# Kernel optimization log

Measured on AMD Instinct MI355X. Metric: run time of the kernel, lower is better.

The kernel has to match this reference:

```python
import jax, jax.numpy as jnp
import numpy as np

B, L, H, HEADS, BLOCKS = 4, 256, 256, 4, 2
D = H // HEADS
EPS = 1e-8
NEG = -4294967295.0  # -2**32 + 1


def rmsnorm(x, w):
    return x * jax.lax.rsqrt(jnp.mean(x * x, axis=-1, keepdims=True) + EPS) * w


def split_heads(x):  # [B,L,H] -> [h,B,L,d]
    return x.reshape(B, L, HEADS, D).transpose(2, 0, 1, 3)


def split_heads_tm(x):  # [B,L,L,H] -> [h,B,L,L,d]
    return x.reshape(B, L, L, HEADS, D).transpose(3, 0, 1, 2, 4)


def setup_inputs() -> dict:
    key = jax.random.key(0)
    ks = jax.random.split(key, 24)
    s = 0.02
    inp = {
        "seqs": jax.random.normal(ks[0], (B, L, H), jnp.float32),
        "attention_mask": jnp.triu(jnp.ones((L, L), jnp.bool_), k=1),  # causal: True = masked
        "timeline_mask": jnp.zeros((B, L), jnp.bool_),
        "time_matrix_K": jax.random.normal(ks[1], (B, L, L, H), jnp.float32),
        "time_matrix_V": jax.random.normal(ks[2], (B, L, L, H), jnp.float32),
        "abs_pos_K": jax.random.normal(ks[3], (B, L, H), jnp.float32),
        "abs_pos_V": jax.random.normal(ks[4], (B, L, H), jnp.float32),
        # parameters, stacked over blocks
        "ln_attn": jnp.ones((BLOCKS, H), jnp.float32),
        "Qw": jax.random.normal(ks[5], (BLOCKS, H, H), jnp.float32) * s,
        "Qb": jnp.zeros((BLOCKS, H), jnp.float32),
        "Kw": jax.random.normal(ks[6], (BLOCKS, H, H), jnp.float32) * s,
        "Kb": jnp.zeros((BLOCKS, H), jnp.float32),
        "Vw": jax.random.normal(ks[7], (BLOCKS, H, H), jnp.float32) * s,
        "Vb": jnp.zeros((BLOCKS, H), jnp.float32),
        "ln_ffn": jnp.ones((BLOCKS, H), jnp.float32),
        "W1": jax.random.normal(ks[8], (BLOCKS, H, H), jnp.float32) * s,
        "b1": jnp.zeros((BLOCKS, H), jnp.float32),
        "W2": jax.random.normal(ks[9], (BLOCKS, H, H), jnp.float32) * s,
        "b2": jnp.zeros((BLOCKS, H), jnp.float32),
        "ln_last": jnp.ones((H,), jnp.float32),
    }
    return inp


def reference(seqs, attention_mask, timeline_mask, time_matrix_K, time_matrix_V,
              abs_pos_K, abs_pos_V, ln_attn, Qw, Qb, Kw, Kb, Vw, Vb,
              ln_ffn, W1, b1, W2, b2, ln_last):
    tmK = split_heads_tm(time_matrix_K)           # [h,B,L,L,d]
    tmV = split_heads_tm(time_matrix_V)
    apK = split_heads(abs_pos_K)                  # [h,B,L,d]
    apV = split_heads(abs_pos_V)
    # True = masked; time_mask masks padded query rows, attn_mask is causal
    mask = timeline_mask[None, :, :, None] | attention_mask[None, None, :, :]  # [1,B,L,L]
    scale = 1.0 / jnp.sqrt(jnp.float32(D))
    not_pad = 1.0 - timeline_mask.astype(seqs.dtype)[:, :, None]  # [B,L,1]

    for i in range(BLOCKS):
        x = rmsnorm(seqs, ln_attn[i])
        Q = split_heads(x @ Qw[i].T + Qb[i])      # queries from normed x
        K = split_heads(seqs @ Kw[i].T + Kb[i])   # keys/values from raw seqs
        V = split_heads(seqs @ Vw[i].T + Vb[i])
        w = jnp.einsum('hbqd,hbkd->hbqk', Q, K)
        w += jnp.einsum('hbqd,hbkd->hbqk', Q, apK)
        w += jnp.einsum('hbqkd,hbqd->hbqk', tmK, Q)
        w = jnp.where(mask, NEG, w * scale)
        A = jax.nn.softmax(w, axis=-1)            # [h,B,L,L]
        out = jnp.einsum('hbqk,hbkd->hbqd', A, V)
        out += jnp.einsum('hbqk,hbkd->hbqd', A, apV)
        out += jnp.einsum('hbqk,hbqkd->hbqd', A, tmV)
        out = out.transpose(1, 2, 0, 3).reshape(B, L, H)  # merge heads
        seqs = seqs + out
        h2 = rmsnorm(seqs, ln_ffn[i])
        ffn = jax.nn.relu(h2 @ W1[i].T + b1[i]) @ W2[i].T + b2[i]
        seqs = (seqs + ffn) * not_pad
    return rmsnorm(seqs, ln_last)
```

## Files before the change

### kernel.cpp

```cpp
#include <hip/hip_runtime.h>
#include <math.h>

#define LLEN 256
#define HDIM 256
#define MM 1024
#define NEGV -4294967295.0f

__device__ __forceinline__ void gemm_core(
    float* A_s, float* W_s, float* r_s,
    const float* __restrict__ A, const float* __restrict__ ln,
    const float* __restrict__ W, const float* __restrict__ bias,
    const float* __restrict__ addv, const float* __restrict__ resid,
    const unsigned char* __restrict__ tl, float* __restrict__ C,
    int relu, int m0, int n0)
{
    int t = threadIdx.x;
    int srow = t >> 4, sc4 = t & 15;
    int tm = t >> 4, tn = t & 15;
    float acc[2][4];
    #pragma unroll
    for (int i = 0; i < 2; ++i)
        #pragma unroll
        for (int j = 0; j < 4; ++j) acc[i][j] = 0.f;
    float ssq[2] = {0.f, 0.f};

    for (int kc = 0; kc < HDIM; kc += 64) {
        #pragma unroll
        for (int i = 0; i < 2; ++i) {
            int row = srow + 16 * i;
            float4 va = *(const float4*)&A[(size_t)(m0 + row) * HDIM + kc + sc4 * 4];
            ssq[i] += va.x*va.x + va.y*va.y + va.z*va.z + va.w*va.w;
            if (ln) {
                va.x *= ln[kc + sc4*4 + 0]; va.y *= ln[kc + sc4*4 + 1];
                va.z *= ln[kc + sc4*4 + 2]; va.w *= ln[kc + sc4*4 + 3];
            }
            *(float4*)&A_s[row * 68 + sc4 * 4] = va;
        }
        #pragma unroll
        for (int i = 0; i < 4; ++i) {
            int row = srow + 16 * i;
            *(float4*)&W_s[row * 68 + sc4 * 4] =
                *(const float4*)&W[(size_t)(n0 + row) * HDIM + kc + sc4 * 4];
        }
        __syncthreads();
        #pragma unroll 4
        for (int k4 = 0; k4 < 16; ++k4) {
            float4 a0 = *(const float4*)&A_s[(2*tm + 0) * 68 + k4 * 4];
            float4 a1 = *(const float4*)&A_s[(2*tm + 1) * 68 + k4 * 4];
            #pragma unroll
            for (int j = 0; j < 4; ++j) {
                float4 wv = *(const float4*)&W_s[(tn + 16*j) * 68 + k4 * 4];
                acc[0][j] = fmaf(a0.x, wv.x, fmaf(a0.y, wv.y,
                            fmaf(a0.z, wv.z, fmaf(a0.w, wv.w, acc[0][j]))));
                acc[1][j] = fmaf(a1.x, wv.x, fmaf(a1.y, wv.y,
                            fmaf(a1.z, wv.z, fmaf(a1.w, wv.w, acc[1][j]))));
            }
        }
        __syncthreads();
    }

    if (ln) {
        #pragma unroll
        for (int i = 0; i < 2; ++i) {
            float v = ssq[i];
            v += __shfl_xor(v, 1); v += __shfl_xor(v, 2);
            v += __shfl_xor(v, 4); v += __shfl_xor(v, 8);
            if (sc4 == 0) r_s[srow + 16 * i] = rsqrtf(v * (1.0f / HDIM) + 1e-8f);
        }
        __syncthreads();
    }

    #pragma unroll
    for (int i = 0; i < 2; ++i) {
        int row = m0 + 2*tm + i;
        float rr = ln ? r_s[2*tm + i] : 1.0f;
        float tlf = tl ? (tl[row] ? 0.f : 1.f) : 1.f;
        #pragma unroll
        for (int j = 0; j < 4; ++j) {
            int col = n0 + tn + 16*j;
            float v = acc[i][j] * rr + bias[col];
            if (relu) v = fmaxf(v, 0.f);
            size_t idx = (size_t)row * HDIM + col;
            if (addv)  v += addv[idx];
            if (resid) v += resid[idx];
            v *= tlf;
            C[idx] = v;
        }
    }
}

__global__ __launch_bounds__(256) void qkv_kernel(
    const float* __restrict__ s, const float* __restrict__ ln_attn,
    const float* __restrict__ Qw, const float* __restrict__ Qb,
    const float* __restrict__ Kw, const float* __restrict__ Kb,
    const float* __restrict__ Vw, const float* __restrict__ Vb,
    const float* __restrict__ apK, const float* __restrict__ apV,
    float* __restrict__ qb, float* __restrict__ kb, float* __restrict__ vb)
{
    __shared__ __align__(16) float A_s[32 * 68];
    __shared__ __align__(16) float W_s[64 * 68];
    __shared__ float r_s[32];
    int m0 = blockIdx.x * 32;
    int sel = blockIdx.y >> 2;
    int n0 = (blockIdx.y & 3) * 64;
    if (sel == 0)
        gemm_core(A_s, W_s, r_s, s, ln_attn, Qw, Qb, nullptr, nullptr, nullptr, qb, 0, m0, n0);
    else if (sel == 1)
        gemm_core(A_s, W_s, r_s, s, nullptr, Kw, Kb, apK, nullptr, nullptr, kb, 0, m0, n0);
    else
        gemm_core(A_s, W_s, r_s, s, nullptr, Vw, Vb, apV, nullptr, nullptr, vb, 0, m0, n0);
}

__global__ __launch_bounds__(256) void gemm_kernel(
    const float* __restrict__ A, const float* __restrict__ ln,
    const float* __restrict__ W, const float* __restrict__ bias,
    const float* __restrict__ resid, const unsigned char* __restrict__ tl,
    float* __restrict__ C, int relu)
{
    __shared__ __align__(16) float A_s[32 * 68];
    __shared__ __align__(16) float W_s[64 * 68];
    __shared__ float r_s[32];
    gemm_core(A_s, W_s, r_s, A, ln, W, bias, nullptr, resid, tl, C, relu,
              blockIdx.x * 32, blockIdx.y * 64);
}

__global__ __launch_bounds__(1024, 8) void attn_kernel(
    const float* __restrict__ Q, const float* __restrict__ Kp,
    const float* __restrict__ Vp, const float* __restrict__ tmK,
    const float* __restrict__ tmV, const unsigned char* __restrict__ tl,
    float* __restrict__ s)
{
    int g = blockIdx.x;
    int b = g >> 7, p = g & 127;
    int tid = threadIdx.x;
    int w = tid >> 6, lane = tid & 63;
    int hh = lane >> 4;

    __shared__ float w_s[4][257];
    __shared__ __align__(16) float out_s[16][256];

    const float4* Kp4 = (const float4*)(Kp + (size_t)b * LLEN * HDIM);
    const float4* Vp4 = (const float4*)(Vp + (size_t)b * LLEN * HDIM);

    for (int rr = 0; rr < 2; ++rr) {
        int q = rr ? (255 - p) : p;
        int bq = b * 256 + q;
        float4 qf = ((const float4*)(Q + (size_t)bq * HDIM))[lane];
        bool tlq = tl[bq] != 0;
        int kmax = tlq ? (LLEN - 1) : q;

        const float4* tmK4 = (const float4*)(tmK + (size_t)bq * LLEN * HDIM);
        const float4* tmV4 = (const float4*)(tmV + (size_t)bq * LLEN * HDIM);

        for (int k = w; k <= kmax; k += 16) {
            float4 kv = Kp4[k * 64 + lane];
            float4 tv = tmK4[k * 64 + lane];
            float sc = qf.x * (kv.x + tv.x) + qf.y * (kv.y + tv.y)
                     + qf.z * (kv.z + tv.z) + qf.w * (kv.w + tv.w);
            sc += __shfl_xor(sc, 1);
            sc += __shfl_xor(sc, 2);
            sc += __shfl_xor(sc, 4);
            sc += __shfl_xor(sc, 8);
            if ((lane & 15) == 0) w_s[lane >> 4][k] = sc;
        }
        __syncthreads();

        if (w < 4) {
            float v0 = w_s[w][lane],       v1 = w_s[w][lane + 64];
            float v2 = w_s[w][lane + 128], v3 = w_s[w][lane + 192];
            v0 = (tlq || (lane       > q)) ? NEGV : v0 * 0.125f;
            v1 = (tlq || (lane + 64  > q)) ? NEGV : v1 * 0.125f;
            v2 = (tlq || (lane + 128 > q)) ? NEGV : v2 * 0.125f;
            v3 = (tlq || (lane + 192 > q)) ? NEGV : v3 * 0.125f;
            float mx = fmaxf(fmaxf(v0, v1), fmaxf(v2, v3));
            #pragma unroll
            for (int m2 = 1; m2 < 64; m2 <<= 1) mx = fmaxf(mx, __shfl_xor(mx, m2));
            float e0 = __expf(v0 - mx), e1 = __expf(v1 - mx);
            float e2 = __expf(v2 - mx), e3 = __expf(v3 - mx);
            float sm = e0 + e1 + e2 + e3;
            #pragma unroll
            for (int m2 = 1; m2 < 64; m2 <<= 1) sm += __shfl_xor(sm, m2);
            float inv = 1.0f / sm;
            w_s[w][lane] = e0 * inv;       w_s[w][lane + 64] = e1 * inv;
            w_s[w][lane + 128] = e2 * inv; w_s[w][lane + 192] = e3 * inv;
        }
        __syncthreads();

        float4 acc = {0.f, 0.f, 0.f, 0.f};
        for (int k = w; k <= kmax; k += 16) {
            float a = w_s[hh][k];
            float4 vv = Vp4[k * 64 + lane];
            float4 tv = tmV4[k * 64 + lane];
            acc.x = fmaf(a, vv.x + tv.x, acc.x);
            acc.y = fmaf(a, vv.y + tv.y, acc.y);
            acc.z = fmaf(a, vv.z + tv.z, acc.z);
            acc.w = fmaf(a, vv.w + tv.w, acc.w);
        }
        *(float4*)&out_s[w][lane * 4] = acc;
        __syncthreads();

        if (tid < 256) {
            float pp = 0.f;
            #pragma unroll
            for (int j = 0; j < 16; ++j) pp += out_s[j][tid];
            s[(size_t)bq * HDIM + tid] += pp;
        }
        __syncthreads();
    }
}

__global__ __launch_bounds__(256) void rmsnorm_kernel(
    const float* __restrict__ x, const float* __restrict__ w, float* __restrict__ y)
{
    int row = blockIdx.x;
    int tid = threadIdx.x;
    float v = x[(size_t)row * HDIM + tid];
    float ss = v * v;
    #pragma unroll
    for (int m = 1; m < 64; m <<= 1) ss += __shfl_xor(ss, m);
    __shared__ float red[4];
    if ((tid & 63) == 0) red[tid >> 6] = ss;
    __syncthreads();
    float tot = red[0] + red[1] + red[2] + red[3];
    float r = rsqrtf(tot * (1.0f / HDIM) + 1e-8f);
    y[(size_t)row * HDIM + tid] = v * r * w[tid];
}

extern "C" void kernel_launch(void* const* d_in, const int* in_sizes, int n_in,
                              void* d_out, int out_size, void* d_ws, size_t ws_size,
                              hipStream_t stream)
{
    const float* seqs = (const float*)d_in[0];
    const unsigned char* tl = (const unsigned char*)d_in[2];
    const float* tmK = (const float*)d_in[3];
    const float* tmV = (const float*)d_in[4];
    const float* apK = (const float*)d_in[5];
    const float* apV = (const float*)d_in[6];
    const float* ln_attn = (const float*)d_in[7];
    const float* Qw = (const float*)d_in[8];
    const float* Qb = (const float*)d_in[9];
    const float* Kw = (const float*)d_in[10];
    const float* Kb = (const float*)d_in[11];
    const float* Vw = (const float*)d_in[12];
    const float* Vb = (const float*)d_in[13];
    const float* ln_ffn = (const float*)d_in[14];
    const float* W1 = (const float*)d_in[15];
    const float* b1 = (const float*)d_in[16];
    const float* W2 = (const float*)d_in[17];
    const float* b2 = (const float*)d_in[18];
    const float* ln_last = (const float*)d_in[19];
    float* out = (float*)d_out;

    const size_t NROW = (size_t)MM * HDIM;
    float* s  = (float*)d_ws;
    float* qb = s  + NROW;
    float* kb = qb + NROW;
    float* vb = kb + NROW;
    float* tb = vb + NROW;

    hipMemcpyAsync(s, seqs, NROW * sizeof(float), hipMemcpyDeviceToDevice, stream);

    for (int i = 0; i < 2; ++i) {
        const float* Qwi = Qw + (size_t)i * HDIM * HDIM;
        const float* Kwi = Kw + (size_t)i * HDIM * HDIM;
        const float* Vwi = Vw + (size_t)i * HDIM * HDIM;
        const float* W1i = W1 + (size_t)i * HDIM * HDIM;
        const float* W2i = W2 + (size_t)i * HDIM * HDIM;

        qkv_kernel<<<dim3(32, 12), 256, 0, stream>>>(
            s, ln_attn + i * HDIM, Qwi, Qb + i * HDIM, Kwi, Kb + i * HDIM,
            Vwi, Vb + i * HDIM, apK, apV, qb, kb, vb);
        attn_kernel<<<512, 1024, 0, stream>>>(qb, kb, vb, tmK, tmV, tl, s);
        gemm_kernel<<<dim3(32, 4), 256, 0, stream>>>(
            s, ln_ffn + i * HDIM, W1i, b1 + i * HDIM, nullptr, nullptr, tb, 1);
        gemm_kernel<<<dim3(32, 4), 256, 0, stream>>>(
            tb, nullptr, W2i, b2 + i * HDIM, s, tl, s, 0);
    }
    rmsnorm_kernel<<<MM, 256, 0, stream>>>(s, ln_last, out);
}
```

Before: 210.8 us.

## Merge attention query pair phases, prefetch K/V loads, enlarge GEMM tiles, drop seqs copy

The attention kernel now processes both paired queries' score passes together with a single softmax phase and fewer barriers. Its K/tmK and V/tmV loops software-prefetch the next row so loads overlap compute. The GEMM tile grows from 32x64 to 64x64 with a 4x4 per-thread micro-tile, raising register reuse but halving block count. The initial device-to-device copy of seqs is removed by reading the input directly on the first block and writing attention output to a separate destination.

```diff
diff --git a/kernel.cpp b/kernel.cpp
--- a/kernel.cpp
+++ b/kernel.cpp
@@ -17,16 +17,16 @@
     int t = threadIdx.x;
     int srow = t >> 4, sc4 = t & 15;
     int tm = t >> 4, tn = t & 15;
-    float acc[2][4];
-    #pragma unroll
-    for (int i = 0; i < 2; ++i)
+    float acc[4][4];
+    #pragma unroll
+    for (int i = 0; i < 4; ++i)
         #pragma unroll
         for (int j = 0; j < 4; ++j) acc[i][j] = 0.f;
-    float ssq[2] = {0.f, 0.f};
+    float ssq[4] = {0.f, 0.f, 0.f, 0.f};
 
     for (int kc = 0; kc < HDIM; kc += 64) {
         #pragma unroll
-        for (int i = 0; i < 2; ++i) {
+        for (int i = 0; i < 4; ++i) {
             int row = srow + 16 * i;
             float4 va = *(const float4*)&A[(size_t)(m0 + row) * HDIM + kc + sc4 * 4];
             ssq[i] += va.x*va.x + va.y*va.y + va.z*va.z + va.w*va.w;
@@ -35,33 +35,32 @@
                 va.z *= ln[kc + sc4*4 + 2]; va.w *= ln[kc + sc4*4 + 3];
             }
             *(float4*)&A_s[row * 68 + sc4 * 4] = va;
-        }
-        #pragma unroll
-        for (int i = 0; i < 4; ++i) {
-            int row = srow + 16 * i;
             *(float4*)&W_s[row * 68 + sc4 * 4] =
                 *(const float4*)&W[(size_t)(n0 + row) * HDIM + kc + sc4 * 4];
         }
         __syncthreads();
         #pragma unroll 4
         for (int k4 = 0; k4 < 16; ++k4) {
-            float4 a0 = *(const float4*)&A_s[(2*tm + 0) * 68 + k4 * 4];
-            float4 a1 = *(const float4*)&A_s[(2*tm + 1) * 68 + k4 * 4];
+            float4 a[4], wv[4];
             #pragma unroll
-            for (int j = 0; j < 4; ++j) {
-                float4 wv = *(const float4*)&W_s[(tn + 16*j) * 68 + k4 * 4];
-                acc[0][j] = fmaf(a0.x, wv.x, fmaf(a0.y, wv.y,
-                            fmaf(a0.z, wv.z, fmaf(a0.w, wv.w, acc[0][j]))));
-                acc[1][j] = fmaf(a1.x, wv.x, fmaf(a1.y, wv.y,
-                            fmaf(a1.z, wv.z, fmaf(a1.w, wv.w, acc[1][j]))));
-            }
+            for (int i = 0; i < 4; ++i)
+                a[i] = *(const float4*)&A_s[(4*tm + i) * 68 + k4 * 4];
+            #pragma unroll
+            for (int j = 0; j < 4; ++j)
+                wv[j] = *(const float4*)&W_s[(tn + 16*j) * 68 + k4 * 4];
+            #pragma unroll
+            for (int i = 0; i < 4; ++i)
+                #pragma unroll
+                for (int j = 0; j < 4; ++j)
+                    acc[i][j] = fmaf(a[i].x, wv[j].x, fmaf(a[i].y, wv[j].y,
+                                fmaf(a[i].z, wv[j].z, fmaf(a[i].w, wv[j].w, acc[i][j]))));
         }
         __syncthreads();
     }
 
     if (ln) {
         #pragma unroll
-        for (int i = 0; i < 2; ++i) {
+        for (int i = 0; i < 4; ++i) {
             float v = ssq[i];
             v += __shfl_xor(v, 1); v += __shfl_xor(v, 2);
             v += __shfl_xor(v, 4); v += __shfl_xor(v, 8);
@@ -71,9 +70,9 @@
     }
 
     #pragma unroll
-    for (int i = 0; i < 2; ++i) {
-        int row = m0 + 2*tm + i;
-        float rr = ln ? r_s[2*tm + i] : 1.0f;
+    for (int i = 0; i < 4; ++i) {
+        int row = m0 + 4*tm + i;
+        float rr = ln ? r_s[4*tm + i] : 1.0f;
         float tlf = tl ? (tl[row] ? 0.f : 1.f) : 1.f;
         #pragma unroll
         for (int j = 0; j < 4; ++j) {
@@ -97,10 +96,10 @@
     const float* __restrict__ apK, const float* __restrict__ apV,
     float* __restrict__ qb, float* __restrict__ kb, float* __restrict__ vb)
 {
-    __shared__ __align__(16) float A_s[32 * 68];
+    __shared__ __align__(16) float A_s[64 * 68];
     __shared__ __align__(16) float W_s[64 * 68];
-    __shared__ float r_s[32];
-    int m0 = blockIdx.x * 32;
+    __shared__ float r_s[64];
+    int m0 = blockIdx.x * 64;
     int sel = blockIdx.y >> 2;
     int n0 = (blockIdx.y & 3) * 64;
     if (sel == 0)
@@ -117,18 +116,18 @@
     const float* __restrict__ resid, const unsigned char* __restrict__ tl,
     float* __restrict__ C, int relu)
 {
-    __shared__ __align__(16) float A_s[32 * 68];
+    __shared__ __align__(16) float A_s[64 * 68];
     __shared__ __align__(16) float W_s[64 * 68];
-    __shared__ float r_s[32];
+    __shared__ float r_s[64];
     gemm_core(A_s, W_s, r_s, A, ln, W, bias, nullptr, resid, tl, C, relu,
-              blockIdx.x * 32, blockIdx.y * 64);
+              blockIdx.x * 64, blockIdx.y * 64);
 }
 
 __global__ __launch_bounds__(1024, 8) void attn_kernel(
     const float* __restrict__ Q, const float* __restrict__ Kp,
     const float* __restrict__ Vp, const float* __restrict__ tmK,
     const float* __restrict__ tmV, const unsigned char* __restrict__ tl,
-    float* __restrict__ s)
+    const float* __restrict__ src, float* __restrict__ dst)
 {
     int g = blockIdx.x;
     int b = g >> 7, p = g & 127;
@@ -136,76 +135,121 @@
     int w = tid >> 6, lane = tid & 63;
     int hh = lane >> 4;
 
-    __shared__ float w_s[4][257];
+    __shared__ float w_s[2][4][257];
     __shared__ __align__(16) float out_s[16][256];
+
+    int q0 = p, q1 = 255 - p;
+    int bq0 = b * 256 + q0, bq1 = b * 256 + q1;
+    float4 qf0 = ((const float4*)(Q + (size_t)bq0 * HDIM))[lane];
+    float4 qf1 = ((const float4*)(Q + (size_t)bq1 * HDIM))[lane];
+    bool tl0 = tl[bq0] != 0, tl1 = tl[bq1] != 0;
+    int kmax0 = tl0 ? (LLEN - 1) : q0;
+    int kmax1 = tl1 ? (LLEN - 1) : q1;
 
     const float4* Kp4 = (const float4*)(Kp + (size_t)b * LLEN * HDIM);
     const float4* Vp4 = (const float4*)(Vp + (size_t)b * LLEN * HDIM);
-
+    const float4* tmK0 = (const float4*)(tmK + (size_t)bq0 * LLEN * HDIM);
+    const float4* tmK1 = (const float4*)(tmK + (size_t)bq1 * LLEN * HDIM);
+    const float4* tmV0 = (const float4*)(tmV + (size_t)bq0 * LLEN * HDIM);
+    const float4* tmV1 = (const float4*)(tmV + (size_t)bq1 * LLEN * HDIM);
+
+    #pragma unroll
     for (int rr = 0; rr < 2; ++rr) {
-        int q = rr ? (255 - p) : p;
-        int bq = b * 256 + q;
-        float4 qf = ((const float4*)(Q + (size_t)bq * HDIM))[lane];
-        bool tlq = tl[bq] != 0;
-        int kmax = tlq ? (LLEN - 1) : q;
-
-        const float4* tmK4 = (const float4*)(tmK + (size_t)bq * LLEN * HDIM);
-        const float4* tmV4 = (const float4*)(tmV + (size_t)bq * LLEN * HDIM);
-
-        for (int k = w; k <= kmax; k += 16) {
+        int kmax = rr ? kmax1 : kmax0;
+        const float4* tmK4 = rr ? tmK1 : tmK0;
+        float4 qf = rr ? qf1 : qf0;
+        int k = w;
+        if (k <= kmax) {
             float4 kv = Kp4[k * 64 + lane];
             float4 tv = tmK4[k * 64 + lane];
-            float sc = qf.x * (kv.x + tv.x) + qf.y * (kv.y + tv.y)
-                     + qf.z * (kv.z + tv.z) + qf.w * (kv.w + tv.w);
-            sc += __shfl_xor(sc, 1);
-            sc += __shfl_xor(sc, 2);
-            sc += __shfl_xor(sc, 4);
-            sc += __shfl_xor(sc, 8);
-            if ((lane & 15) == 0) w_s[lane >> 4][k] = sc;
-        }
-        __syncthreads();
-
-        if (w < 4) {
-            float v0 = w_s[w][lane],       v1 = w_s[w][lane + 64];
-            float v2 = w_s[w][lane + 128], v3 = w_s[w][lane + 192];
-            v0 = (tlq || (lane       > q)) ? NEGV : v0 * 0.125f;
-            v1 = (tlq || (lane + 64  > q)) ? NEGV : v1 * 0.125f;
-            v2 = (tlq || (lane + 128 > q)) ? NEGV : v2 * 0.125f;
-            v3 = (tlq || (lane + 192 > q)) ? NEGV : v3 * 0.125f;
-            float mx = fmaxf(fmaxf(v0, v1), fmaxf(v2, v3));
-            #pragma unroll
-            for (int m2 = 1; m2 < 64; m2 <<= 1) mx = fmaxf(mx, __shfl_xor(mx, m2));
-            float e0 = __expf(v0 - mx), e1 = __expf(v1 - mx);
-            float e2 = __expf(v2 - mx), e3 = __expf(v3 - mx);
-            float sm = e0 + e1 + e2 + e3;
-            #pragma unroll
-            for (int m2 = 1; m2 < 64; m2 <<= 1) sm += __shfl_xor(sm, m2);
-            float inv = 1.0f / sm;
-            w_s[w][lane] = e0 * inv;       w_s[w][lane + 64] = e1 * inv;
-            w_s[w][lane + 128] = e2 * inv; w_s[w][lane + 192] = e3 * inv;
-        }
-        __syncthreads();
-
+            while (true) {
+                int kn = k + 16;
+                bool more = (kn <= kmax);
+                float4 kv2, tv2;
+                if (more) { kv2 = Kp4[kn * 64 + lane]; tv2 = tmK4[kn * 64 + lane]; }
+                float sc = qf.x * (kv.x + tv.x) + qf.y * (kv.y + tv.y)
+                         + qf.z * (kv.z + tv.z) + qf.w * (kv.w + tv.w);
+                sc += __shfl_xor(sc, 1);
+                sc += __shfl_xor(sc, 2);
+                sc += __shfl_xor(sc, 4);
+                sc += __shfl_xor(sc, 8);
+                if ((lane & 15) == 0) w_s[rr][lane >> 4][k] = sc;
+                if (!more) break;
+                kv = kv2; tv = tv2; k = kn;
+            }
+        }
+    }
+    __syncthreads();
+
+    if (w < 8) {
+        int r = w >> 2, h = w & 3;
+        int q = r ? q1 : q0;
+        bool tlq = r ? tl1 : tl0;
+        float v0 = w_s[r][h][lane],       v1 = w_s[r][h][lane + 64];
+        float v2 = w_s[r][h][lane + 128], v3 = w_s[r][h][lane + 192];
+        v0 = (tlq || (lane       > q)) ? NEGV : v0 * 0.125f;
+        v1 = (tlq || (lane + 64  > q)) ? NEGV : v1 * 0.125f;
+        v2 = (tlq || (lane + 128 > q)) ? NEGV : v2 * 0.125f;
+        v3 = (tlq || (lane + 192 > q)) ? NEGV : v3 * 0.125f;
+        float mx = fmaxf(fmaxf(v0, v1), fmaxf(v2, v3));
+        #pragma unroll
+        for (int m2 = 1; m2 < 64; m2 <<= 1) mx = fmaxf(mx, __shfl_xor(mx, m2));
+        float e0 = __expf(v0 - mx), e1 = __expf(v1 - mx);
+        float e2 = __expf(v2 - mx), e3 = __expf(v3 - mx);
+        float sm = e0 + e1 + e2 + e3;
+        #pragma unroll
+        for (int m2 = 1; m2 < 64; m2 <<= 1) sm += __shfl_xor(sm, m2);
+        float inv = 1.0f / sm;
+        w_s[r][h][lane] = e0 * inv;       w_s[r][h][lane + 64] = e1 * inv;
+        w_s[r][h][lane + 128] = e2 * inv; w_s[r][h][lane + 192] = e3 * inv;
+    }
+    __syncthreads();
+
+    float4 acc0 = {0.f, 0.f, 0.f, 0.f}, acc1 = {0.f, 0.f, 0.f, 0.f};
+    #pragma unroll
+    for (int rr = 0; rr < 2; ++rr) {
+        int kmax = rr ? kmax1 : kmax0;
+        const float4* tmV4 = rr ? tmV1 : tmV0;
         float4 acc = {0.f, 0.f, 0.f, 0.f};
-        for (int k = w; k <= kmax; k += 16) {
-            float a = w_s[hh][k];
+        int k = w;
+        if (k <= kmax) {
             float4 vv = Vp4[k * 64 + lane];
             float4 tv = tmV4[k * 64 + lane];
-            acc.x = fmaf(a, vv.x + tv.x, acc.x);
-            acc.y = fmaf(a, vv.y + tv.y, acc.y);
-            acc.z = fmaf(a, vv.z + tv.z, acc.z);
-            acc.w = fmaf(a, vv.w + tv.w, acc.w);
-        }
-        *(float4*)&out_s[w][lane * 4] = acc;
-        __syncthreads();
-
-        if (tid < 256) {
-            float pp = 0.f;
-            #pragma unroll
-            for (int j = 0; j < 16; ++j) pp += out_s[j][tid];
-            s[(size_t)bq * HDIM + tid] += pp;
-        }
-        __syncthreads();
+            while (true) {
+                int kn = k + 16;
+                bool more = (kn <= kmax);
+                float4 vv2, tv2;
+                if (more) { vv2 = Vp4[kn * 64 + lane]; tv2 = tmV4[kn * 64 + lane]; }
+                float a = w_s[rr][hh][k];
+                acc.x = fmaf(a, vv.x + tv.x, acc.x);
+                acc.y = fmaf(a, vv.y + tv.y, acc.y);
+                acc.z = fmaf(a, vv.z + tv.z, acc.z);
+                acc.w = fmaf(a, vv.w + tv.w, acc.w);
+                if (!more) break;
+                vv = vv2; tv = tv2; k = kn;
+            }
+        }
+        if (rr) acc1 = acc; else acc0 = acc;
+    }
+
+    *(float4*)&out_s[w][lane * 4] = acc0;
+    __syncthreads();
+    if (tid < 256) {
+        float pp = 0.f;
+        #pragma unroll
+        for (int j = 0; j < 16; ++j) pp += out_s[j][tid];
+        size_t idx = (size_t)bq0 * HDIM + tid;
+        dst[idx] = src[idx] + pp;
+    }
+    __syncthreads();
+    *(float4*)&out_s[w][lane * 4] = acc1;
+    __syncthreads();
+    if (tid < 256) {
+        float pp = 0.f;
+        #pragma unroll
+        for (int j = 0; j < 16; ++j) pp += out_s[j][tid];
+        size_t idx = (size_t)bq1 * HDIM + tid;
+        dst[idx] = src[idx] + pp;
     }
 }
 
@@ -258,22 +302,21 @@
     float* vb = kb + NROW;
     float* tb = vb + NROW;
 
-    hipMemcpyAsync(s, seqs, NROW * sizeof(float), hipMemcpyDeviceToDevice, stream);
-
     for (int i = 0; i < 2; ++i) {
         const float* Qwi = Qw + (size_t)i * HDIM * HDIM;
         const float* Kwi = Kw + (size_t)i * HDIM * HDIM;
         const float* Vwi = Vw + (size_t)i * HDIM * HDIM;
         const float* W1i = W1 + (size_t)i * HDIM * HDIM;
         const float* W2i = W2 + (size_t)i * HDIM * HDIM;
-
-        qkv_kernel<<<dim3(32, 12), 256, 0, stream>>>(
-            s, ln_attn + i * HDIM, Qwi, Qb + i * HDIM, Kwi, Kb + i * HDIM,
+        const float* cur = (i == 0) ? seqs : s;
+
+        qkv_kernel<<<dim3(16, 12), 256, 0, stream>>>(
+            cur, ln_attn + i * HDIM, Qwi, Qb + i * HDIM, Kwi, Kb + i * HDIM,
             Vwi, Vb + i * HDIM, apK, apV, qb, kb, vb);
-        attn_kernel<<<512, 1024, 0, stream>>>(qb, kb, vb, tmK, tmV, tl, s);
-        gemm_kernel<<<dim3(32, 4), 256, 0, stream>>>(
+        attn_kernel<<<512, 1024, 0, stream>>>(qb, kb, vb, tmK, tmV, tl, cur, s);
+        gemm_kernel<<<dim3(16, 4), 256, 0, stream>>>(
             s, ln_ffn + i * HDIM, W1i, b1 + i * HDIM, nullptr, nullptr, tb, 1);
-        gemm_kernel<<<dim3(32, 4), 256, 0, stream>>>(
+        gemm_kernel<<<dim3(16, 4), 256, 0, stream>>>(
             tb, nullptr, W2i, b2 + i * HDIM, s, tl, s, 0);
     }
     rmsnorm_kernel<<<MM, 256, 0, stream>>>(s, ln_last, out);
```

New measurement: 238.3 us. 13.0% more time.

## Fuse attention score and value passes with online softmax per warp

Applied to the files above, without the earlier changes.

Replaces the two-pass attention (scores, then a block-wide softmax, then a separate V pass) with a single pass. Each warp keeps a running max and sum (online softmax) and accumulates V plus time-matrix V in the same loop, and per-warp partials are merged at the end with rescaling. This removes a block barrier and a second sweep over K/V indices, and lets the tmK and tmV loads be issued together. It also drops the initial device-to-device copy by reading the input sequence directly in block 0 and writing the residual into the workspace. The cost is extra exp calls per key.

```diff
diff --git a/kernel.cpp b/kernel.cpp
--- a/kernel.cpp
+++ b/kernel.cpp
@@ -128,7 +128,7 @@
     const float* __restrict__ Q, const float* __restrict__ Kp,
     const float* __restrict__ Vp, const float* __restrict__ tmK,
     const float* __restrict__ tmV, const unsigned char* __restrict__ tl,
-    float* __restrict__ s)
+    const float* __restrict__ src, float* __restrict__ dst)
 {
     int g = blockIdx.x;
     int b = g >> 7, p = g & 127;
@@ -136,12 +136,13 @@
     int w = tid >> 6, lane = tid & 63;
     int hh = lane >> 4;
 
-    __shared__ float w_s[4][257];
     __shared__ __align__(16) float out_s[16][256];
+    __shared__ float m_s[16][4], l_s[16][4];
 
     const float4* Kp4 = (const float4*)(Kp + (size_t)b * LLEN * HDIM);
     const float4* Vp4 = (const float4*)(Vp + (size_t)b * LLEN * HDIM);
 
+    #pragma unroll
     for (int rr = 0; rr < 2; ++rr) {
         int q = rr ? (255 - p) : p;
         int bq = b * 256 + q;
@@ -152,58 +153,51 @@
         const float4* tmK4 = (const float4*)(tmK + (size_t)bq * LLEN * HDIM);
         const float4* tmV4 = (const float4*)(tmV + (size_t)bq * LLEN * HDIM);
 
+        float4 acc = {0.f, 0.f, 0.f, 0.f};
+        float m = -INFINITY, l = 0.f;
+
         for (int k = w; k <= kmax; k += 16) {
-            float4 kv = Kp4[k * 64 + lane];
-            float4 tv = tmK4[k * 64 + lane];
-            float sc = qf.x * (kv.x + tv.x) + qf.y * (kv.y + tv.y)
-                     + qf.z * (kv.z + tv.z) + qf.w * (kv.w + tv.w);
-            sc += __shfl_xor(sc, 1);
-            sc += __shfl_xor(sc, 2);
-            sc += __shfl_xor(sc, 4);
-            sc += __shfl_xor(sc, 8);
-            if ((lane & 15) == 0) w_s[lane >> 4][k] = sc;
-        }
-        __syncthreads();
-
-        if (w < 4) {
-            float v0 = w_s[w][lane],       v1 = w_s[w][lane + 64];
-            float v2 = w_s[w][lane + 128], v3 = w_s[w][lane + 192];
-            v0 = (tlq || (lane       > q)) ? NEGV : v0 * 0.125f;
-            v1 = (tlq || (lane + 64  > q)) ? NEGV : v1 * 0.125f;
-            v2 = (tlq || (lane + 128 > q)) ? NEGV : v2 * 0.125f;
-            v3 = (tlq || (lane + 192 > q)) ? NEGV : v3 * 0.125f;
-            float mx = fmaxf(fmaxf(v0, v1), fmaxf(v2, v3));
+            int off = k * 64 + lane;
+            float4 kv = Kp4[off];
+            float4 tv = tmK4[off];
+            float4 vv = Vp4[off];
+            float4 tw = tmV4[off];
+            float s = qf.x * (kv.x + tv.x) + qf.y * (kv.y + tv.y)
+                    + qf.z * (kv.z + tv.z) + qf.w * (kv.w + tv.w);
+            s += __shfl_xor(s, 1);
+            s += __shfl_xor(s, 2);
+            s += __shfl_xor(s, 4);
+            s += __shfl_xor(s, 8);
+            s = tlq ? NEGV : s * 0.125f;
+            float mn = fmaxf(m, s);
+            float c = __expf(m - mn);
+            float e = __expf(s - mn);
+            l = l * c + e;
+            acc.x = fmaf(acc.x, c, e * (vv.x + tw.x));
+            acc.y = fmaf(acc.y, c, e * (vv.y + tw.y));
+            acc.z = fmaf(acc.z, c, e * (vv.z + tw.z));
+            acc.w = fmaf(acc.w, c, e * (vv.w + tw.w));
+            m = mn;
+        }
+
+        if ((lane & 15) == 0) { m_s[w][hh] = m; l_s[w][hh] = l; }
+        *(float4*)&out_s[w][lane * 4] = acc;
+        __syncthreads();
+
+        if (tid < 256) {
+            int h = tid >> 6;
+            float mt = -INFINITY;
             #pragma unroll
-            for (int m2 = 1; m2 < 64; m2 <<= 1) mx = fmaxf(mx, __shfl_xor(mx, m2));
-            float e0 = __expf(v0 - mx), e1 = __expf(v1 - mx);
-            float e2 = __expf(v2 - mx), e3 = __expf(v3 - mx);
-            float sm = e0 + e1 + e2 + e3;
+            for (int j = 0; j < 16; ++j) mt = fmaxf(mt, m_s[j][h]);
+            float lt = 0.f, o = 0.f;
             #pragma unroll
-            for (int m2 = 1; m2 < 64; m2 <<= 1) sm += __shfl_xor(sm, m2);
-            float inv = 1.0f / sm;
-            w_s[w][lane] = e0 * inv;       w_s[w][lane + 64] = e1 * inv;
-            w_s[w][lane + 128] = e2 * inv; w_s[w][lane + 192] = e3 * inv;
-        }
-        __syncthreads();
-
-        float4 acc = {0.f, 0.f, 0.f, 0.f};
-        for (int k = w; k <= kmax; k += 16) {
-            float a = w_s[hh][k];
-            float4 vv = Vp4[k * 64 + lane];
-            float4 tv = tmV4[k * 64 + lane];
-            acc.x = fmaf(a, vv.x + tv.x, acc.x);
-            acc.y = fmaf(a, vv.y + tv.y, acc.y);
-            acc.z = fmaf(a, vv.z + tv.z, acc.z);
-            acc.w = fmaf(a, vv.w + tv.w, acc.w);
-        }
-        *(float4*)&out_s[w][lane * 4] = acc;
-        __syncthreads();
-
-        if (tid < 256) {
-            float pp = 0.f;
-            #pragma unroll
-            for (int j = 0; j < 16; ++j) pp += out_s[j][tid];
-            s[(size_t)bq * HDIM + tid] += pp;
+            for (int j = 0; j < 16; ++j) {
+                float f = __expf(m_s[j][h] - mt);
+                lt = fmaf(l_s[j][h], f, lt);
+                o  = fmaf(out_s[j][tid], f, o);
+            }
+            size_t idx = (size_t)bq * HDIM + tid;
+            dst[idx] = src[idx] + o / lt;
         }
         __syncthreads();
     }
@@ -258,19 +252,18 @@
     float* vb = kb + NROW;
     float* tb = vb + NROW;
 
-    hipMemcpyAsync(s, seqs, NROW * sizeof(float), hipMemcpyDeviceToDevice, stream);
-
     for (int i = 0; i < 2; ++i) {
         const float* Qwi = Qw + (size_t)i * HDIM * HDIM;
         const float* Kwi = Kw + (size_t)i * HDIM * HDIM;
         const float* Vwi = Vw + (size_t)i * HDIM * HDIM;
         const float* W1i = W1 + (size_t)i * HDIM * HDIM;
         const float* W2i = W2 + (size_t)i * HDIM * HDIM;
+        const float* cur = (i == 0) ? seqs : s;
 
         qkv_kernel<<<dim3(32, 12), 256, 0, stream>>>(
-            s, ln_attn + i * HDIM, Qwi, Qb + i * HDIM, Kwi, Kb + i * HDIM,
+            cur, ln_attn + i * HDIM, Qwi, Qb + i * HDIM, Kwi, Kb + i * HDIM,
             Vwi, Vb + i * HDIM, apK, apV, qb, kb, vb);
-        attn_kernel<<<512, 1024, 0, stream>>>(qb, kb, vb, tmK, tmV, tl, s);
+        attn_kernel<<<512, 1024, 0, stream>>>(qb, kb, vb, tmK, tmV, tl, cur, s);
         gemm_kernel<<<dim3(32, 4), 256, 0, stream>>>(
             s, ln_ffn + i * HDIM, W1i, b1 + i * HDIM, nullptr, nullptr, tb, 1);
         gemm_kernel<<<dim3(32, 4), 256, 0, stream>>>(
```

After: 202.0 us (median of 2 runs). 4.2% less time.
